# Kernel tuning notes

Hardware: AMD Instinct MI355X
Metric: run time of the kernel (lower is better)

The kernel has to match this reference:

```python
import jax, jax.numpy as jnp
import numpy as np

B, T, M, S = 16384, 128, 4, 12  # num_series, timesteps, measurements, states


def setup_inputs() -> dict:
    key = jax.random.key(0)
    ks = jax.random.split(key, 7)
    inp = jax.random.normal(ks[0], (B, T, M), dtype=jnp.float32)
    # stable transition matrix near identity
    F = jnp.eye(S, dtype=jnp.float32) + 0.05 * jax.random.normal(ks[1], (S, S), dtype=jnp.float32) / np.float32(np.sqrt(S))
    H = jax.random.normal(ks[2], (M, S), dtype=jnp.float32) / np.float32(np.sqrt(S))
    Aq = 0.1 * jax.random.normal(ks[3], (S, S), dtype=jnp.float32)
    Q = Aq @ Aq.T + 1e-3 * jnp.eye(S, dtype=jnp.float32)  # PSD process noise
    Ar = 0.1 * jax.random.normal(ks[4], (M, M), dtype=jnp.float32)
    R = Ar @ Ar.T + 1e-3 * jnp.eye(M, dtype=jnp.float32)  # PSD measurement noise
    m0 = jax.random.normal(ks[5], (B, S, 1), dtype=jnp.float32)
    Ap = 0.1 * jax.random.normal(ks[6], (B, S, S), dtype=jnp.float32)
    P0 = jnp.einsum('bij,bkj->bik', Ap, Ap) + 1e-2 * jnp.eye(S, dtype=jnp.float32)
    return {"inp": inp, "F": F, "H": H, "Q": Q, "R": R, "m0": m0, "P0": P0}


def _kalman_forward(inp, F, H, Q, R, m0, P0):
    I_S = jnp.eye(S, dtype=inp.dtype)
    # t = -1 step of the original loop: one predict from the initial state
    m = jnp.einsum('ij,bjk->bik', F, m0)                      # [B,S,1]
    P = jnp.einsum('ij,bjk,lk->bil', F, P0, F) + Q            # [B,S,S]

    def step(carry, obs_t):
        m, P = carry  # one-step-ahead prior at time t
        y = jnp.einsum('ms,bsk->bmk', H, m)                   # predicted measurement [B,M,1]
        # --- kf_update ---
        resid = obs_t - y[..., 0]                             # [B,M]
        Sm = jnp.einsum('ms,bst,nt->bmn', H, P, H) + R        # innovation cov [B,M,M]
        Sinv = jnp.linalg.inv(Sm)
        K = jnp.einsum('bst,mt,bmn->bsn', P, H, Sinv)         # Kalman gain [B,S,M]
        m_f = m + jnp.einsum('bsm,bm->bs', K, resid)[..., None]
        ImKH = I_S - jnp.einsum('bsm,mt->bst', K, H)
        # Joseph stabilized covariance update
        P_f = (jnp.einsum('bij,bjk,blk->bil', ImKH, P, ImKH)
               + jnp.einsum('bim,mn,bjn->bij', K, R, K))
        # --- kf_predict for next timestep ---
        m_n = jnp.einsum('ij,bjk->bik', F, m_f)
        P_n = jnp.einsum('ij,bjk,lk->bil', F, P_f, F) + Q
        return (m_n, P_n), y

    _, ys = jax.lax.scan(step, (m, P), jnp.swapaxes(inp, 0, 1))  # ys: [T,B,M,1]
    # original forward does torch.cat(predicted_measurements, 0) -> [T*B, M, 1]
    return ys.reshape(T * B, M, 1)


def reference(inp, F, H, Q, R, m0, P0):
    return _kalman_forward(inp, F, H, Q, R, m0, P0)
```

## Files before the change

kernel.cpp:

```cpp
#include <hip/hip_runtime.h>

#define BN 16384
#define TT 128
#define MM 4
#define SS 12
#define BLOCK 64
#define NSER (BLOCK / 4)
#define TSTRIDE 145

__global__ __launch_bounds__(BLOCK, 1) void kf_kernel(
    const float* __restrict__ inp,
    const float* __restrict__ Fm,
    const float* __restrict__ Hm,
    const float* __restrict__ Qm,
    const float* __restrict__ Rm,
    const float* __restrict__ m0p,
    const float* __restrict__ P0p,
    float* __restrict__ outp)
{
    __shared__ double Fd[SS * SS];
    __shared__ double Hd[MM * SS];
    __shared__ double Qd[SS * SS];
    __shared__ double Rd[MM * MM];
    __shared__ double tb[NSER * TSTRIDE];

    const int tid  = threadIdx.x;
    const int gid  = blockIdx.x * BLOCK + tid;
    const int b    = gid >> 2;
    const int c    = gid & 3;
    const int sb   = tid >> 2;
    const int col0 = 3 * c;

    for (int i = tid; i < SS * SS; i += BLOCK) {
        Fd[i] = (double)Fm[i];
        Qd[i] = (double)Qm[i];
    }
    if (tid < MM * SS) Hd[tid] = (double)Hm[tid];
    if (tid < MM * MM) Rd[tid] = (double)Rm[tid];

    double m[SS];
#pragma unroll
    for (int s = 0; s < SS; ++s) m[s] = (double)m0p[b * SS + s];

    double P[SS][3];
#pragma unroll
    for (int s = 0; s < SS; ++s)
#pragma unroll
        for (int jj = 0; jj < 3; ++jj)
            P[s][jj] = (double)P0p[b * SS * SS + s * SS + col0 + jj];

    const float* op = inp + b * (TT * MM) + c;
    float obn = op[0];
    double* tser = &tb[sb * TSTRIDE];

    __syncthreads();

#pragma unroll 1
    for (int t = 0; t < TT; ++t) {
        double mv[SS];
        __syncthreads();
#pragma unroll
        for (int i = 0; i < SS; ++i) {
            double fr[SS];
#pragma unroll
            for (int s = 0; s < SS; ++s) fr[s] = Fd[i * SS + s];
            double a = 0.0, u0 = 0.0, u1 = 0.0, u2 = 0.0;
#pragma unroll
            for (int s = 0; s < SS; ++s) {
                a  += fr[s] * m[s];
                u0 += fr[s] * P[s][0];
                u1 += fr[s] * P[s][1];
                u2 += fr[s] * P[s][2];
            }
            mv[i] = a;
            tser[i * SS + col0 + 0] = u0;
            tser[i * SS + col0 + 1] = u1;
            tser[i * SS + col0 + 2] = u2;
        }
        __syncthreads();

#pragma unroll
        for (int h = 0; h < 2; ++h) {
            double Ur[3][6];
#pragma unroll
            for (int jj = 0; jj < 3; ++jj)
#pragma unroll
                for (int kk = 0; kk < 6; ++kk)
                    Ur[jj][kk] = tser[(col0 + jj) * SS + h * 6 + kk];
#pragma unroll
            for (int s = 0; s < SS; ++s) {
                double fr6[6];
#pragma unroll
                for (int kk = 0; kk < 6; ++kk) fr6[kk] = Fd[s * SS + h * 6 + kk];
                double p0 = (h == 0) ? Qd[s * SS + col0 + 0] : P[s][0];
                double p1 = (h == 0) ? Qd[s * SS + col0 + 1] : P[s][1];
                double p2 = (h == 0) ? Qd[s * SS + col0 + 2] : P[s][2];
#pragma unroll
                for (int kk = 0; kk < 6; ++kk) {
                    p0 += Ur[0][kk] * fr6[kk];
                    p1 += Ur[1][kk] * fr6[kk];
                    p2 += Ur[2][kk] * fr6[kk];
                }
                P[s][0] = p0; P[s][1] = p1; P[s][2] = p2;
            }
        }

        double y = 0.0;
#pragma unroll
        for (int s = 0; s < SS; ++s) y += Hd[c * SS + s] * mv[s];
        outp[t * (BN * MM) + b * MM + c] = (float)y;

        float obc = obn;
        if (t + 1 < TT) obn = op[(t + 1) * MM];

        double rc = (double)obc - y;
        double r0 = __shfl(rc, 0, 4), r1 = __shfl(rc, 1, 4);
        double r2 = __shfl(rc, 2, 4), r3 = __shfl(rc, 3, 4);

        double HPl[MM][3];
#pragma unroll
        for (int n = 0; n < MM; ++n) {
            double h0 = 0.0, h1 = 0.0, h2 = 0.0;
#pragma unroll
            for (int s = 0; s < SS; ++s) {
                double hv = Hd[n * SS + s];
                h0 += hv * P[s][0]; h1 += hv * P[s][1]; h2 += hv * P[s][2];
            }
            HPl[n][0] = h0; HPl[n][1] = h1; HPl[n][2] = h2;
        }

        double Su[10];
        {
            int u = 0;
#pragma unroll
            for (int n = 0; n < MM; ++n)
#pragma unroll
                for (int t2 = n; t2 < MM; ++t2) {
                    double acc = HPl[n][0] * Hd[t2 * SS + col0 + 0]
                               + HPl[n][1] * Hd[t2 * SS + col0 + 1]
                               + HPl[n][2] * Hd[t2 * SS + col0 + 2];
                    acc += __shfl_xor(acc, 1, 4);
                    acc += __shfl_xor(acc, 2, 4);
                    Su[u++] = acc + Rd[n * MM + t2];
                }
        }
        double s00 = Su[0], s01 = Su[1], s02 = Su[2], s03 = Su[3];
        double s11 = Su[4], s12 = Su[5], s13 = Su[6];
        double s22 = Su[7], s23 = Su[8], s33 = Su[9];

        double ra   = 1.0 / (s00 * s11 - s01 * s01);
        double ai00 = s11 * ra, ai01 = -s01 * ra, ai11 = s00 * ra;
        double w00 = ai00 * s02 + ai01 * s12;
        double w01 = ai00 * s03 + ai01 * s13;
        double w10 = ai01 * s02 + ai11 * s12;
        double w11 = ai01 * s03 + ai11 * s13;
        double e00 = s22 - (s02 * w00 + s12 * w10);
        double e01 = s23 - (s02 * w01 + s12 * w11);
        double e11 = s33 - (s03 * w01 + s13 * w11);
        double rmm = 1.0 / (e00 * e11 - e01 * e01);
        double q22 = e11 * rmm, q23 = -e01 * rmm, q33 = e00 * rmm;
        double x00 = w00 * q22 + w01 * q23;
        double x01 = w00 * q23 + w01 * q33;
        double x10 = w10 * q22 + w11 * q23;
        double x11 = w10 * q23 + w11 * q33;
        double q00 = ai00 + x00 * w00 + x01 * w01;
        double q01 = ai01 + x00 * w10 + x01 * w11;
        double q11 = ai11 + x10 * w10 + x11 * w11;
        double Qi[MM][MM] = {
            { q00,  q01,  -x00, -x01 },
            { q01,  q11,  -x10, -x11 },
            { -x00, -x10,  q22,  q23 },
            { -x01, -x11,  q23,  q33 }
        };

        double z0 = Qi[0][0] * r0 + Qi[0][1] * r1 + Qi[0][2] * r2 + Qi[0][3] * r3;
        double z1 = Qi[1][0] * r0 + Qi[1][1] * r1 + Qi[1][2] * r2 + Qi[1][3] * r3;
        double z2 = Qi[2][0] * r0 + Qi[2][1] * r1 + Qi[2][2] * r2 + Qi[2][3] * r3;
        double z3 = Qi[3][0] * r0 + Qi[3][1] * r1 + Qi[3][2] * r2 + Qi[3][3] * r3;

        double upd[3];
#pragma unroll
        for (int jj = 0; jj < 3; ++jj)
            upd[jj] = HPl[0][jj] * z0 + HPl[1][jj] * z1
                    + HPl[2][jj] * z2 + HPl[3][jj] * z3;

#pragma unroll
        for (int k = 0; k < SS; ++k)
            m[k] = __shfl(mv[k] + upd[k % 3], k / 3, 4);

        double G[MM][3];
#pragma unroll
        for (int n = 0; n < MM; ++n)
#pragma unroll
            for (int jj = 0; jj < 3; ++jj)
                G[n][jj] = Qi[n][0] * HPl[0][jj] + Qi[n][1] * HPl[1][jj]
                         + Qi[n][2] * HPl[2][jj] + Qi[n][3] * HPl[3][jj];

#pragma unroll
        for (int s = 0; s < SS; ++s) {
            double h0 = __shfl(HPl[0][s % 3], s / 3, 4);
            double h1 = __shfl(HPl[1][s % 3], s / 3, 4);
            double h2 = __shfl(HPl[2][s % 3], s / 3, 4);
            double h3 = __shfl(HPl[3][s % 3], s / 3, 4);
#pragma unroll
            for (int jj = 0; jj < 3; ++jj)
                P[s][jj] -= h0 * G[0][jj] + h1 * G[1][jj]
                          + h2 * G[2][jj] + h3 * G[3][jj];
        }
    }
}

extern "C" void kernel_launch(void* const* d_in, const int* in_sizes, int n_in,
                              void* d_out, int out_size, void* d_ws, size_t ws_size,
                              hipStream_t stream) {
    const float* inp = (const float*)d_in[0];
    const float* F   = (const float*)d_in[1];
    const float* H   = (const float*)d_in[2];
    const float* Q   = (const float*)d_in[3];
    const float* R   = (const float*)d_in[4];
    const float* m0  = (const float*)d_in[5];
    const float* P0  = (const float*)d_in[6];
    float* out = (float*)d_out;

    dim3 grid((BN * MM) / BLOCK), block(BLOCK);
    hipLaunchKernelGGL(kf_kernel, grid, block, 0, stream,
                       inp, F, H, Q, R, m0, P0, out);
}
```

Measured before the change: 912.4 us.

## Cache H, Q, R in registers, split mean predict across lanes, use wave barriers

Moves H, the per-lane Q columns and the upper triangle of R from shared memory into registers. Each lane now computes only its 3 predicted-mean components, and the predicted measurement is assembled with quad shuffles instead of every lane computing all 12 components. The block-wide __syncthreads are replaced by wave barriers, since the 64-thread block is a single wavefront. This cuts redundant mean FLOPs and LDS traffic but raises register pressure, which could spill in the double-precision code.

```diff
diff --git a/kernel.cpp b/kernel.cpp
--- a/kernel.cpp
+++ b/kernel.cpp
@@ -7,6 +7,7 @@
 #define BLOCK 64
 #define NSER (BLOCK / 4)
 #define TSTRIDE 145
+
 
 __global__ __launch_bounds__(BLOCK, 1) void kf_kernel(
     const float* __restrict__ inp,
@@ -19,9 +20,6 @@
     float* __restrict__ outp)
 {
     __shared__ double Fd[SS * SS];
-    __shared__ double Hd[MM * SS];
-    __shared__ double Qd[SS * SS];
-    __shared__ double Rd[MM * MM];
     __shared__ double tb[NSER * TSTRIDE];
 
     const int tid  = threadIdx.x;
@@ -31,12 +29,35 @@
     const int sb   = tid >> 2;
     const int col0 = 3 * c;
 
-    for (int i = tid; i < SS * SS; i += BLOCK) {
-        Fd[i] = (double)Fm[i];
-        Qd[i] = (double)Qm[i];
+    for (int i = tid; i < SS * SS; i += BLOCK) Fd[i] = (double)Fm[i];
+
+    double Hf[MM][SS];
+#pragma unroll
+    for (int n = 0; n < MM; ++n)
+#pragma unroll
+        for (int s = 0; s < SS; ++s) Hf[n][s] = (double)Hm[n * SS + s];
+
+    double Hc[MM][3];
+#pragma unroll
+    for (int n = 0; n < MM; ++n)
+#pragma unroll
+        for (int jj = 0; jj < 3; ++jj) Hc[n][jj] = (double)Hm[n * SS + col0 + jj];
+
+    double Rs[10];
+    {
+        int u = 0;
+#pragma unroll
+        for (int n = 0; n < MM; ++n)
+#pragma unroll
+            for (int t2 = 0; t2 < MM; ++t2)
+                if (t2 >= n) Rs[u++] = (double)Rm[n * MM + t2];
     }
-    if (tid < MM * SS) Hd[tid] = (double)Hm[tid];
-    if (tid < MM * MM) Rd[tid] = (double)Rm[tid];
+
+    double Qc[SS][3];
+#pragma unroll
+    for (int s = 0; s < SS; ++s)
+#pragma unroll
+        for (int jj = 0; jj < 3; ++jj) Qc[s][jj] = (double)Qm[s * SS + col0 + jj];
 
     double m[SS];
 #pragma unroll
@@ -57,27 +78,34 @@
 
 #pragma unroll 1
     for (int t = 0; t < TT; ++t) {
-        double mv[SS];
-        __syncthreads();
+        __builtin_amdgcn_wave_barrier();
 #pragma unroll
         for (int i = 0; i < SS; ++i) {
             double fr[SS];
 #pragma unroll
             for (int s = 0; s < SS; ++s) fr[s] = Fd[i * SS + s];
-            double a = 0.0, u0 = 0.0, u1 = 0.0, u2 = 0.0;
+            double u0 = 0.0, u1 = 0.0, u2 = 0.0;
 #pragma unroll
             for (int s = 0; s < SS; ++s) {
-                a  += fr[s] * m[s];
                 u0 += fr[s] * P[s][0];
                 u1 += fr[s] * P[s][1];
                 u2 += fr[s] * P[s][2];
             }
-            mv[i] = a;
             tser[i * SS + col0 + 0] = u0;
             tser[i * SS + col0 + 1] = u1;
             tser[i * SS + col0 + 2] = u2;
         }
-        __syncthreads();
+
+        double mvl[3];
+#pragma unroll
+        for (int jj = 0; jj < 3; ++jj) {
+            double a = 0.0;
+#pragma unroll
+            for (int s = 0; s < SS; ++s) a += Fd[(col0 + jj) * SS + s] * m[s];
+            mvl[jj] = a;
+        }
+
+        __builtin_amdgcn_wave_barrier();
 
 #pragma unroll
         for (int h = 0; h < 2; ++h) {
@@ -92,9 +120,9 @@
                 double fr6[6];
 #pragma unroll
                 for (int kk = 0; kk < 6; ++kk) fr6[kk] = Fd[s * SS + h * 6 + kk];
-                double p0 = (h == 0) ? Qd[s * SS + col0 + 0] : P[s][0];
-                double p1 = (h == 0) ? Qd[s * SS + col0 + 1] : P[s][1];
-                double p2 = (h == 0) ? Qd[s * SS + col0 + 2] : P[s][2];
+                double p0 = (h == 0) ? Qc[s][0] : P[s][0];
+                double p1 = (h == 0) ? Qc[s][1] : P[s][1];
+                double p2 = (h == 0) ? Qc[s][2] : P[s][2];
 #pragma unroll
                 for (int kk = 0; kk < 6; ++kk) {
                     p0 += Ur[0][kk] * fr6[kk];
@@ -105,17 +133,24 @@
             }
         }
 
-        double y = 0.0;
-#pragma unroll
-        for (int s = 0; s < SS; ++s) y += Hd[c * SS + s] * mv[s];
-        outp[t * (BN * MM) + b * MM + c] = (float)y;
+        double y[MM];
+#pragma unroll
+        for (int n = 0; n < MM; ++n) {
+            double py = Hc[n][0] * mvl[0] + Hc[n][1] * mvl[1] + Hc[n][2] * mvl[2];
+            py += __shfl_xor(py, 1, 4);
+            py += __shfl_xor(py, 2, 4);
+            y[n] = py;
+        }
+        double ysel = (c & 2) ? ((c & 1) ? y[3] : y[2]) : ((c & 1) ? y[1] : y[0]);
+        outp[t * (BN * MM) + b * MM + c] = (float)ysel;
 
         float obc = obn;
         if (t + 1 < TT) obn = op[(t + 1) * MM];
 
-        double rc = (double)obc - y;
-        double r0 = __shfl(rc, 0, 4), r1 = __shfl(rc, 1, 4);
-        double r2 = __shfl(rc, 2, 4), r3 = __shfl(rc, 3, 4);
+        double r[MM];
+#pragma unroll
+        for (int n = 0; n < MM; ++n)
+            r[n] = (double)__shfl(obc, n, 4) - y[n];
 
         double HPl[MM][3];
 #pragma unroll
@@ -123,7 +158,7 @@
             double h0 = 0.0, h1 = 0.0, h2 = 0.0;
 #pragma unroll
             for (int s = 0; s < SS; ++s) {
-                double hv = Hd[n * SS + s];
+                double hv = Hf[n][s];
                 h0 += hv * P[s][0]; h1 += hv * P[s][1]; h2 += hv * P[s][2];
             }
             HPl[n][0] = h0; HPl[n][1] = h1; HPl[n][2] = h2;
@@ -135,13 +170,15 @@
 #pragma unroll
             for (int n = 0; n < MM; ++n)
 #pragma unroll
-                for (int t2 = n; t2 < MM; ++t2) {
-                    double acc = HPl[n][0] * Hd[t2 * SS + col0 + 0]
-                               + HPl[n][1] * Hd[t2 * SS + col0 + 1]
-                               + HPl[n][2] * Hd[t2 * SS + col0 + 2];
+                for (int t2 = 0; t2 < MM; ++t2) {
+                    if (t2 < n) continue;
+                    double acc = HPl[n][0] * Hc[t2][0]
+                               + HPl[n][1] * Hc[t2][1]
+                               + HPl[n][2] * Hc[t2][2];
                     acc += __shfl_xor(acc, 1, 4);
                     acc += __shfl_xor(acc, 2, 4);
-                    Su[u++] = acc + Rd[n * MM + t2];
+                    Su[u] = acc + Rs[u];
+                    ++u;
                 }
         }
         double s00 = Su[0], s01 = Su[1], s02 = Su[2], s03 = Su[3];
@@ -173,10 +210,10 @@
             { -x01, -x11,  q23,  q33 }
         };
 
-        double z0 = Qi[0][0] * r0 + Qi[0][1] * r1 + Qi[0][2] * r2 + Qi[0][3] * r3;
-        double z1 = Qi[1][0] * r0 + Qi[1][1] * r1 + Qi[1][2] * r2 + Qi[1][3] * r3;
-        double z2 = Qi[2][0] * r0 + Qi[2][1] * r1 + Qi[2][2] * r2 + Qi[2][3] * r3;
-        double z3 = Qi[3][0] * r0 + Qi[3][1] * r1 + Qi[3][2] * r2 + Qi[3][3] * r3;
+        double z0 = Qi[0][0] * r[0] + Qi[0][1] * r[1] + Qi[0][2] * r[2] + Qi[0][3] * r[3];
+        double z1 = Qi[1][0] * r[0] + Qi[1][1] * r[1] + Qi[1][2] * r[2] + Qi[1][3] * r[3];
+        double z2 = Qi[2][0] * r[0] + Qi[2][1] * r[1] + Qi[2][2] * r[2] + Qi[2][3] * r[3];
+        double z3 = Qi[3][0] * r[0] + Qi[3][1] * r[1] + Qi[3][2] * r[2] + Qi[3][3] * r[3];
 
         double upd[3];
 #pragma unroll
@@ -186,7 +223,7 @@
 
 #pragma unroll
         for (int k = 0; k < SS; ++k)
-            m[k] = __shfl(mv[k] + upd[k % 3], k / 3, 4);
+            m[k] = __shfl(mvl[k % 3] + upd[k % 3], k / 3, 4);
 
         double G[MM][3];
 #pragma unroll
```

Result: slower. 1.401 ms (+53.5%).
